# Kernel tuning notes

Hardware: AMD Instinct MI355X
Metric: run time of the kernel (lower is better)

Reference implementation:

```python
import jax, jax.numpy as jnp
import numpy as np

N_P, N_I, DIM = 30, 40, 6
W_I, C1, C2, LAM = 0.7, 1.5, 1.5, 0.3
EPS = 1e-8


def _decode(pos):
    # pos: [P, 6] -> per-particle fusion weights via pairwise softmax
    e = jnp.exp(pos[:, :4])
    fg_s = e[:, 0] + e[:, 1] + EPS
    bg_s = e[:, 2] + e[:, 3] + EPS
    return e[:, 0] / fg_s, e[:, 1] / fg_s, e[:, 2] / bg_s, e[:, 3] / bg_s


def _fitness(pos, rgb, dep, mask, r_dep):
    # rgb, dep, mask, r_dep: [H, W]; pos: [P, 6] -> scores [P]
    rgb_fg, dep_fg, rgb_bg, dep_bg = _decode(pos)
    mn = mask - mask.mean()
    mn_norm = jnp.linalg.norm(mn) + EPS
    fg = rgb_fg[:, None, None] * rgb + dep_fg[:, None, None] * dep   # [P,H,W]
    bg = rgb_bg[:, None, None] * rgb + dep_bg[:, None, None] * dep
    fused = mask * fg + (1.0 - mask) * bg
    fn = fused - fused.mean(axis=(1, 2), keepdims=True)
    fn_norm = jnp.sqrt((fn * fn).sum(axis=(1, 2)))
    ncc = (fn * mn).sum(axis=(1, 2)) / (fn_norm * mn_norm + EPS)
    pen_fg = ((1.0 - r_dep) * mask).mean()
    pen_bg = ((1.0 - r_dep) * (1.0 - mask)).mean()
    rel_pen = dep_fg * pen_fg + dep_bg * pen_bg
    return ncc - LAM * rel_pen


def _pso(rgb, dep, mask, r_dep):
    # Deterministic PSO with fixed RNG key; inputs are [H, W] maps.
    key = jax.random.key(42)
    k_pos, k_vel, k_r1, k_r2 = jax.random.split(key, 4)
    pos = jax.random.uniform(k_pos, (N_P, DIM), minval=-2.0, maxval=2.0)
    vel = jax.random.uniform(k_vel, (N_P, DIM), minval=-0.5, maxval=0.5)
    r1s = jax.random.uniform(k_r1, (N_I, N_P, DIM))
    r2s = jax.random.uniform(k_r2, (N_I, N_P, DIM))

    pb_pos = pos
    pb_fit = _fitness(pos, rgb, dep, mask, r_dep)
    gi = jnp.argmax(pb_fit)
    gb_pos = pb_pos[gi]
    gb_fit = pb_fit[gi]

    def step(carry, rs):
        pos, vel, pb_pos, pb_fit, gb_pos, gb_fit = carry
        r1, r2 = rs
        vel = W_I * vel + C1 * r1 * (pb_pos - pos) + C2 * r2 * (gb_pos - pos)
        pos = jnp.clip(pos + vel, -3.0, 3.0)
        fit = _fitness(pos, rgb, dep, mask, r_dep)
        better = fit > pb_fit
        pb_pos = jnp.where(better[:, None], pos, pb_pos)
        pb_fit = jnp.where(better, fit, pb_fit)
        bi = jnp.argmax(pb_fit)
        improve = pb_fit[bi] > gb_fit
        gb_pos = jnp.where(improve, pb_pos[bi], gb_pos)
        gb_fit = jnp.where(improve, pb_fit[bi], gb_fit)
        return (pos, vel, pb_pos, pb_fit, gb_pos, gb_fit), None

    (pos, vel, pb_pos, pb_fit, gb_pos, gb_fit), _ = jax.lax.scan(
        step, (pos, vel, pb_pos, pb_fit, gb_pos, gb_fit), (r1s, r2s))
    rgb_fg, dep_fg, rgb_bg, dep_bg = _decode(gb_pos[None, :])
    return rgb_fg[0], dep_fg[0], rgb_bg[0], dep_bg[0]


def _cos_sim(feat, proto):
    # feat [B,C,H,W], proto [B,C] -> [B,H,W]; matches F.normalize (clamp_min eps)
    p = proto / jnp.maximum(jnp.linalg.norm(proto, axis=1, keepdims=True), 1e-12)
    fnorm = jnp.maximum(jnp.sqrt((feat * feat).sum(axis=1, keepdims=True)), 1e-12)
    f = feat / fnorm
    return jnp.einsum('bchw,bc->bhw', f, p)


def setup_inputs() -> dict:
    key = jax.random.key(0)
    ks = jax.random.split(key, 10)
    B, C, H, W = 8, 256, 64, 64
    return {
        'f_rgb': jax.random.normal(ks[0], (B, C, H, W), dtype=jnp.float32),
        'f_depth': jax.random.normal(ks[1], (B, C, H, W), dtype=jnp.float32),
        'r_rgb': jax.random.uniform(ks[2], (B, 1, H, W), dtype=jnp.float32),
        'r_depth': jax.random.uniform(ks[3], (B, 1, H, W), dtype=jnp.float32),
        'proto_rgb': jax.random.normal(ks[4], (B, C), dtype=jnp.float32),
        'proto_dep': jax.random.normal(ks[5], (B, C), dtype=jnp.float32),
        'query_mask': jax.random.uniform(ks[6], (B, 1, H, W), dtype=jnp.float32),
        'conv_w': jax.random.normal(ks[7], (C, C), dtype=jnp.float32) * 0.05,
        'bn_gamma': jax.random.uniform(ks[8], (C,), dtype=jnp.float32),
        'bn_beta': jax.random.normal(ks[9], (C,), dtype=jnp.float32) * 0.1,
        'bn_mean': jnp.zeros((C,), dtype=jnp.float32),
        'bn_var': jnp.ones((C,), dtype=jnp.float32),
    }


def reference(f_rgb, f_depth, r_rgb, r_depth, proto_rgb, proto_dep, query_mask,
              conv_w, bn_gamma, bn_beta, bn_mean, bn_var):
    # cosine similarity maps [B,H,W]
    rgb_sim = _cos_sim(f_rgb, proto_rgb)
    dep_sim = _cos_sim(f_depth, proto_dep)

    # PSO operates on detached batch-mean maps (torch .detach().mean(0).cpu())
    sg = jax.lax.stop_gradient
    np_rgb = sg(rgb_sim).mean(axis=0)                 # [H,W]
    np_dep = sg(dep_sim).mean(axis=0)                 # [H,W]
    np_mask = sg(query_mask)[:, 0].mean(axis=0)       # mask already at (H,W): nearest interp is identity
    np_r_dep = sg(r_depth)[:, 0].mean(axis=0)
    rgb_fg, dep_fg, rgb_bg, dep_bg = _pso(np_rgb, np_dep, np_mask, np_r_dep)

    f_fg = rgb_fg * f_rgb + dep_fg * f_depth
    f_bg = rgb_bg * f_rgb + dep_bg * f_depth
    proxy = jax.nn.sigmoid((rgb_sim + dep_sim)[:, None] * 3.0)   # [B,1,H,W]
    f_fused = proxy * f_fg + (1.0 - proxy) * f_bg

    # post_proj: 1x1 conv (no bias) -> BN (eval) -> ReLU
    y = jnp.einsum('oc,bchw->bohw', conv_w, f_fused)
    inv = bn_gamma / jnp.sqrt(bn_var + 1e-5)
    y = y * inv[None, :, None, None] + (bn_beta - bn_mean * inv)[None, :, None, None]
    return jax.nn.relu(y)
```

## Files before the change

### kernel.cpp

```cpp
#include <hip/hip_runtime.h>
#include <stdint.h>
#include <float.h>

static constexpr size_t WS_SIM_RGB = 4096;
static constexpr size_t WS_SIM_DEP = 36864;
static constexpr size_t WS_NPMAPS  = 69632;
static constexpr size_t WS_SYNC    = 86048;
static constexpr size_t WS_RNG     = 90112;

typedef short short8 __attribute__((ext_vector_type(8)));
typedef float f32x4 __attribute__((ext_vector_type(4)));

static constexpr uint32_t SYNC_MAGIC = 0x5A17C0DEu;

__device__ __forceinline__ uint32_t pack_bf2(float a, float b) {
  uint32_t ua = __float_as_uint(a), ub = __float_as_uint(b);
  uint32_t ra = (ua + 0x7fffu + ((ua >> 16) & 1u)) >> 16;
  uint32_t rb = (ub + 0x7fffu + ((ub >> 16) & 1u)) >> 16;
  return (ra & 0xffffu) | (rb << 16);
}

__device__ __forceinline__ void threefry2x32(uint32_t k0, uint32_t k1,
                                             uint32_t c0, uint32_t c1,
                                             uint32_t& o0, uint32_t& o1) {
  uint32_t ks2 = k0 ^ k1 ^ 0x1BD11BDAu;
  uint32_t x0 = c0 + k0;
  uint32_t x1 = c1 + k1;
#define TF_ROUND(r) { x0 += x1; x1 = (x1 << (r)) | (x1 >> (32 - (r))); x1 ^= x0; }
  TF_ROUND(13) TF_ROUND(15) TF_ROUND(26) TF_ROUND(6)
  x0 += k1;  x1 += ks2 + 1u;
  TF_ROUND(17) TF_ROUND(29) TF_ROUND(16) TF_ROUND(24)
  x0 += ks2; x1 += k0 + 2u;
  TF_ROUND(13) TF_ROUND(15) TF_ROUND(26) TF_ROUND(6)
  x0 += k0;  x1 += k1 + 3u;
  TF_ROUND(17) TF_ROUND(29) TF_ROUND(16) TF_ROUND(24)
  x0 += k1;  x1 += ks2 + 4u;
  TF_ROUND(13) TF_ROUND(15) TF_ROUND(26) TF_ROUND(6)
  x0 += ks2; x1 += k0 + 5u;
#undef TF_ROUND
  o0 = x0; o1 = x1;
}

__device__ __forceinline__ float tf_u01(uint32_t k0, uint32_t k1, uint32_t idx) {
  uint32_t o0, o1;
  threefry2x32(k0, k1, 0u, idx, o0, o1);
  uint32_t bits = o0 ^ o1;
  uint32_t fb = (bits >> 9) | 0x3F800000u;
  return __uint_as_float(fb) - 1.0f;
}

__global__ __launch_bounds__(256) void sim_kernel(
    const float* __restrict__ f_rgb, const float* __restrict__ f_dep,
    const float* __restrict__ proto_rgb, const float* __restrict__ proto_dep,
    float* __restrict__ sim_rgb, float* __restrict__ sim_dep) {
  int tid = threadIdx.x;
  int bm = blockIdx.y;
  int b = bm >> 1, mo = bm & 1;
  const float* f  = mo ? f_dep : f_rgb;
  const float* pr = mo ? proto_dep : proto_rgb;
  float* sim = mo ? sim_dep : sim_rgb;
  __shared__ float shp[256];
  __shared__ float wsum[4];
  float pv = pr[b * 256 + tid];
  float ss0 = pv * pv;
#pragma unroll
  for (int off = 32; off > 0; off >>= 1) ss0 += __shfl_xor(ss0, off, 64);
  if ((tid & 63) == 0) wsum[tid >> 6] = ss0;
  __syncthreads();
  float nrm = fmaxf(sqrtf(wsum[0] + wsum[1] + wsum[2] + wsum[3]), 1e-12f);
  shp[tid] = pv / nrm;
  __syncthreads();
  int p = blockIdx.x * 256 + tid;
  const float* base = f + (size_t)b * 256 * 4096 + p;
  float dot = 0.f, ss = 0.f;
#pragma unroll 8
  for (int c = 0; c < 256; ++c) {
    float x = base[(size_t)c * 4096];
    dot += x * shp[c];
    ss  += x * x;
  }
  float fn = fmaxf(sqrtf(ss), 1e-12f);
  sim[b * 4096 + p] = dot / fn;
}

__global__ __launch_bounds__(256) void npmaps_kernel(
    const float* __restrict__ sim_rgb, const float* __restrict__ sim_dep,
    const float* __restrict__ qmask, const float* __restrict__ r_dep,
    float* __restrict__ npm) {
  int i = blockIdx.x * 256 + threadIdx.x;
  float sr = 0.f, sd = 0.f, sm = 0.f, sq = 0.f;
#pragma unroll
  for (int b = 0; b < 8; ++b) {
    sr += sim_rgb[b * 4096 + i];
    sd += sim_dep[b * 4096 + i];
    sm += qmask[b * 4096 + i];
    sq += r_dep[b * 4096 + i];
  }
  npm[i]          = sr * 0.125f;
  npm[4096 + i]   = sd * 0.125f;
  npm[8192 + i]   = sm * 0.125f;
  npm[12288 + i]  = sq * 0.125f;
}

__global__ __launch_bounds__(256) void rng_kernel(float* __restrict__ rng) {
  int g = blockIdx.x * 256 + threadIdx.x;
  if (g >= 14760) return;
  int kind; uint32_t splitIdx, ctr, dst;
  if (g < 180) {
    kind = 0; splitIdx = 0; ctr = (uint32_t)g; dst = (uint32_t)g;
  } else if (g < 360) {
    kind = 1; splitIdx = 1; ctr = (uint32_t)(g - 180); dst = (uint32_t)g;
  } else if (g < 7560) {
    uint32_t c = (uint32_t)(g - 360);
    kind = 2; splitIdx = 2; ctr = c;
    uint32_t t = c / 180u, rem = c % 180u, p = rem / 6u, d = rem % 6u;
    dst = 360u + t * 360u + p * 12u + d;
  } else {
    uint32_t c = (uint32_t)(g - 7560);
    kind = 3; splitIdx = 3; ctr = c;
    uint32_t t = c / 180u, rem = c % 180u, p = rem / 6u, d = rem % 6u;
    dst = 360u + t * 360u + p * 12u + 6u + d;
  }
  uint32_t k0, k1;
  threefry2x32(0u, 42u, 0u, splitIdx, k0, k1);
  float u = tf_u01(k0, k1, ctr);
  float v;
  if (kind == 0)      v = fmaxf(-2.0f, u * 4.0f - 2.0f);
  else if (kind == 1) v = fmaxf(-0.5f, u - 0.5f);
  else                v = u;
  rng[dst] = v;
}

__device__ __forceinline__ float pso_fitness_fast(const float pos[6],
    const float S[4], const float G[16], const float V[4],
    float mn_norm, float pen_fg, float pen_bg) {
  float e0 = __expf(pos[0]), e1 = __expf(pos[1]);
  float e2 = __expf(pos[2]), e3 = __expf(pos[3]);
  float rf = __builtin_amdgcn_rcpf(e0 + e1 + 1e-8f);
  float rb = __builtin_amdgcn_rcpf(e2 + e3 + 1e-8f);
  float w[4] = {e0 * rf, e1 * rf, e2 * rb, e3 * rb};
  float num = 0.f, mus = 0.f;
#pragma unroll
  for (int k = 0; k < 4; ++k) { num += w[k] * V[k]; mus += w[k] * S[k]; }
  float q = 0.f;
#pragma unroll
  for (int j = 0; j < 4; ++j)
#pragma unroll
    for (int k = 0; k < 4; ++k) q += w[j] * G[j * 4 + k] * w[k];
  float fn2 = fmaxf(q - mus * mus * (1.f / 4096.f), 0.f);
  float den = __builtin_amdgcn_sqrtf(fn2) * mn_norm + 1e-8f;
  float ncc = num * __builtin_amdgcn_rcpf(den);
  return ncc - 0.3f * (w[1] * pen_fg + w[3] * pen_bg);
}

__device__ __forceinline__ float wavemax_lo32(float v) {
  int x = __float_as_int(v);
#define DPP_STEP(ctrl) { \
    int y = __builtin_amdgcn_update_dpp(x, x, ctrl, 0xf, 0xf, false); \
    x = __float_as_int(fmaxf(__int_as_float(x), __int_as_float(y))); }
  DPP_STEP(0x128)
  DPP_STEP(0x124)
  DPP_STEP(0x122)
  DPP_STEP(0x121)
#undef DPP_STEP
  float r0 = __int_as_float(__builtin_amdgcn_readlane(x, 0));
  float r1 = __int_as_float(__builtin_amdgcn_readlane(x, 16));
  return fmaxf(r0, r1);
}

__global__ __launch_bounds__(256, 4) void mega_kernel(
    const float* __restrict__ f_rgb, const float* __restrict__ f_dep,
    const float* __restrict__ sim_rgb, const float* __restrict__ sim_dep,
    const float* __restrict__ npm, const float* __restrict__ rng,
    const float* __restrict__ W,
    const float* __restrict__ bn_g, const float* __restrict__ bn_b,
    const float* __restrict__ bn_m, const float* __restrict__ bn_v,
    uint32_t* __restrict__ sync, float* __restrict__ out) {
  __shared__ __align__(16) uint32_t smem[4736];
  const int tid = threadIdx.x;
  const int bid = blockIdx.x;

  if (bid == 0) {
    float* colf = (float*)smem;
    float* res1 = colf + 17 * 257;
    float* res2 = res1 + 17;
    float* sst  = res2 + 5;
    const float* np_rgb  = npm;
    const float* np_dep  = npm + 4096;
    const float* np_mask = npm + 8192;
    const float* np_rdep = npm + 12288;
    {
      float acc[17];
#pragma unroll
      for (int k = 0; k < 17; ++k) acc[k] = 0.f;
      for (int i = tid; i < 4096; i += 256) {
        float m = np_mask[i], r = np_rgb[i], d = np_dep[i], q = np_rdep[i];
        float om = 1.f - m;
        float M1 = m * r, M2 = m * d, M3 = om * r, M4 = om * d;
        acc[0] += m;
        acc[1] += M1; acc[2] += M2; acc[3] += M3; acc[4] += M4;
        acc[5] += M1 * M1; acc[6] += M1 * M2; acc[7] += M1 * M3; acc[8] += M1 * M4;
        acc[9] += M2 * M2; acc[10] += M2 * M3; acc[11] += M2 * M4;
        acc[12] += M3 * M3; acc[13] += M3 * M4; acc[14] += M4 * M4;
        float oq = 1.f - q;
        acc[15] += oq * m; acc[16] += oq * om;
      }
#pragma unroll
      for (int k = 0; k < 17; ++k) colf[k * 257 + tid] = acc[k];
      __syncthreads();
      if (tid < 17) { float s = 0.f; for (int i = 0; i < 256; ++i) s += colf[tid * 257 + i]; res1[tid] = s; }
      __syncthreads();
      float mask_mean = res1[0] * (1.f / 4096.f);
      float a2[5] = {0.f, 0.f, 0.f, 0.f, 0.f};
      for (int i = tid; i < 4096; i += 256) {
        float m = np_mask[i], r = np_rgb[i], d = np_dep[i];
        float om = 1.f - m;
        float mn = m - mask_mean;
        a2[0] += m * r * mn; a2[1] += m * d * mn;
        a2[2] += om * r * mn; a2[3] += om * d * mn;
        a2[4] += mn * mn;
      }
      __syncthreads();
#pragma unroll
      for (int k = 0; k < 5; ++k) colf[k * 257 + tid] = a2[k];
      __syncthreads();
      if (tid < 5) { float s = 0.f; for (int i = 0; i < 256; ++i) s += colf[tid * 257 + i]; res2[tid] = s; }
      __syncthreads();
      if (tid == 0) {
        sst[0] = res1[1]; sst[1] = res1[2]; sst[2] = res1[3]; sst[3] = res1[4];
        float G11 = res1[5], G12 = res1[6], G13 = res1[7], G14 = res1[8];
        float G22 = res1[9], G23 = res1[10], G24 = res1[11];
        float G33 = res1[12], G34 = res1[13], G44 = res1[14];
        float Gf[16] = {G11, G12, G13, G14,  G12, G22, G23, G24,
                        G13, G23, G33, G34,  G14, G24, G34, G44};
        for (int k = 0; k < 16; ++k) sst[4 + k] = Gf[k];
        sst[20] = res2[0]; sst[21] = res2[1]; sst[22] = res2[2]; sst[23] = res2[3];
        sst[24] = sqrtf(res2[4]) + 1e-8f;
        sst[25] = res1[15] * (1.f / 4096.f);
        sst[26] = res1[16] * (1.f / 4096.f);
      }
      __syncthreads();
    }
    if (tid >= 64) return;
    int lane = tid;
    bool act = lane < 30;
    float S[4], G[16], V[4];
#pragma unroll
    for (int k = 0; k < 4; ++k) S[k] = sst[k];
#pragma unroll
    for (int k = 0; k < 16; ++k) G[k] = sst[4 + k];
#pragma unroll
    for (int k = 0; k < 4; ++k) V[k] = sst[20 + k];
    float mn_norm = sst[24], pen_fg = sst[25], pen_bg = sst[26];

    float pos[6], vel[6], pbp[6];
#pragma unroll
    for (int d = 0; d < 6; ++d) { pos[d] = 0.f; vel[d] = 0.f; }
    if (act) {
#pragma unroll
      for (int d = 0; d < 6; ++d) {
        pos[d] = rng[lane * 6 + d];
        vel[d] = rng[180 + lane * 6 + d];
      }
    }
#pragma unroll
    for (int d = 0; d < 6; ++d) pbp[d] = pos[d];

    float f0 = pso_fitness_fast(pos, S, G, V, mn_norm, pen_fg, pen_bg);
    float pbf = act ? f0 : -FLT_MAX;

    float gbf = wavemax_lo32(pbf);
    float gb[6];
    {
      unsigned long long mm = __ballot(pbf == gbf);
      int bl = __ffsll(mm) - 1;
#pragma unroll
      for (int d = 0; d < 6; ++d)
        gb[d] = __int_as_float(__builtin_amdgcn_readlane(__float_as_int(pbp[d]), bl));
    }

    const float* rbase = rng + 360;
    float4 A0, A1, A2, B0, B1, B2;
    {
      const float4* p0 = (const float4*)(rbase + lane * 12);
      A0 = p0[0]; A1 = p0[1]; A2 = p0[2];
      const float4* p1 = (const float4*)(rbase + 360 + lane * 12);
      B0 = p1[0]; B1 = p1[1]; B2 = p1[2];
    }

#define PSO_ITER(R0, R1, R2, TNEXT) { \
    float r1v[6] = {R0.x, R0.y, R0.z, R0.w, R1.x, R1.y}; \
    float r2v[6] = {R1.z, R1.w, R2.x, R2.y, R2.z, R2.w}; \
    const float4* pf = (const float4*)(rbase + (TNEXT) * 360 + lane * 12); \
    R0 = pf[0]; R1 = pf[1]; R2 = pf[2]; \
    _Pragma("unroll") \
    for (int d = 0; d < 6; ++d) { \
      vel[d] = 0.7f * vel[d] + 1.5f * r1v[d] * (pbp[d] - pos[d]) \
                             + 1.5f * r2v[d] * (gb[d] - pos[d]); \
      pos[d] = fmaxf(-3.0f, fminf(pos[d] + vel[d], 3.0f)); \
    } \
    float f = pso_fitness_fast(pos, S, G, V, mn_norm, pen_fg, pen_bg); \
    if (act && f > pbf) { \
      pbf = f; \
      _Pragma("unroll") for (int d = 0; d < 6; ++d) pbp[d] = pos[d]; \
    } \
    float maxv = wavemax_lo32(pbf); \
    if (maxv > gbf) {     \
      unsigned long long mm = __ballot(pbf == maxv); \
      int bl = __ffsll(mm) - 1; \
      gbf = maxv; \
      _Pragma("unroll") for (int d = 0; d < 6; ++d) \
        gb[d] = __int_as_float(__builtin_amdgcn_readlane(__float_as_int(pbp[d]), bl)); \
    } \
  }

    for (int k = 0; k < 20; ++k) {
      PSO_ITER(A0, A1, A2, 2 * k + 2)
      PSO_ITER(B0, B1, B2, 2 * k + 3)
    }
#undef PSO_ITER

    if (lane == 0) {
      float e0 = expf(gb[0]), e1 = expf(gb[1]), e2 = expf(gb[2]), e3 = expf(gb[3]);
      float fgs = e0 + e1 + 1e-8f, bgs = e2 + e3 + 1e-8f;
      uint32_t u0 = __float_as_uint(e0 / fgs);
      uint32_t u1 = __float_as_uint(e1 / fgs);
      uint32_t u2 = __float_as_uint(e2 / bgs);
      uint32_t u3 = __float_as_uint(e3 / bgs);
      atomicExch(&sync[0], u0);
      atomicExch(&sync[1], u1);
      atomicExch(&sync[2], u2);
      atomicExch(&sync[3], u3);
      __threadfence();
      atomicExch(&sync[4], u0 ^ u1 ^ u2 ^ u3 ^ SYNC_MAGIC);
    }
    return;
  }

  uint32_t* As = smem;
  uint32_t* BR = smem + 2560;
  uint32_t* BD = smem + 3648;
  const int gi = bid - 1;
  const int t0 = gi;
  const int t1 = (gi == 0) ? 1023 : -1;

  const int n4 = (tid & 15) * 4, kp = tid >> 4;
  const int am = tid & 127, kh = tid >> 7;
  const int lane = tid & 63, wv = tid >> 6;
  const int wm = wv >> 1, wn = wv & 1;
  const int lg = lane >> 4, ln = lane & 15;

  float pa = 0.f, pb_ = 0.f, pc_ = 0.f, pd_ = 0.f;
  bool have = false;

  for (int pass = 0; pass < 2; ++pass) {
    const int t = pass ? t1 : t0;
    if (t < 0) break;
    const int b = t >> 7, rem = t & 127, mt = rem >> 6, nt = rem & 63;
    const int m0 = mt * 128, n0 = nt * 64;
    const size_t fb = (size_t)b << 20;
    const float* frb = f_rgb + fb + n0 + n4;
    const float* fdb = f_dep + fb + n0 + n4;
    const float* wrow = W + (size_t)(m0 + am) * 256 + kh * 16;

    f32x4 accR[4][2], accD[4][2];
#pragma unroll
    for (int i = 0; i < 4; ++i)
#pragma unroll
      for (int j = 0; j < 2; ++j) { accR[i][j] = (f32x4)0.f; accD[i][j] = (f32x4)0.f; }

    for (int s8 = 0; s8 < 8; ++s8) {
      const int k0 = s8 * 32;
      {
        const size_t ko = (size_t)(k0 + 2 * kp) * 4096;
        const f32x4 r0 = *(const f32x4*)(frb + ko);
        const f32x4 r1 = *(const f32x4*)(frb + ko + 4096);
        const f32x4 d0 = *(const f32x4*)(fdb + ko);
        const f32x4 d1 = *(const f32x4*)(fdb + ko + 4096);
#pragma unroll
        for (int i2 = 0; i2 < 4; ++i2) {
          BR[(n4 + i2) * 17 + kp] = pack_bf2(r0[i2], r1[i2]);
          BD[(n4 + i2) * 17 + kp] = pack_bf2(d0[i2], d1[i2]);
        }
        const f32x4 w0 = *(const f32x4*)(wrow + k0);
        const f32x4 w1 = *(const f32x4*)(wrow + k0 + 4);
        const f32x4 w2 = *(const f32x4*)(wrow + k0 + 8);
        const f32x4 w3 = *(const f32x4*)(wrow + k0 + 12);
        uint32_t* ap = &As[am * 20 + kh * 8];
        ap[0] = pack_bf2(w0[0], w0[1]); ap[1] = pack_bf2(w0[2], w0[3]);
        ap[2] = pack_bf2(w1[0], w1[1]); ap[3] = pack_bf2(w1[2], w1[3]);
        ap[4] = pack_bf2(w2[0], w2[1]); ap[5] = pack_bf2(w2[2], w2[3]);
        ap[6] = pack_bf2(w3[0], w3[1]); ap[7] = pack_bf2(w3[2], w3[3]);
      }
      __syncthreads();
      short8 af[4], bfr[2], bfd[2];
#pragma unroll
      for (int i = 0; i < 4; ++i) {
        int m = wm * 64 + i * 16 + ln;
        float4 tq = *(const float4*)(&As[m * 20 + lg * 4]);
        af[i] = *(short8*)&tq;
      }
#pragma unroll
      for (int j = 0; j < 2; ++j) {
        int n = wn * 32 + j * 16 + ln;
        const uint32_t* bp = &BR[n * 17 + lg * 4];
        union { uint32_t w[4]; short8 v; } u;
        u.w[0] = bp[0]; u.w[1] = bp[1]; u.w[2] = bp[2]; u.w[3] = bp[3];
        bfr[j] = u.v;
        const uint32_t* dp = &BD[n * 17 + lg * 4];
        union { uint32_t w[4]; short8 v; } ud;
        ud.w[0] = dp[0]; ud.w[1] = dp[1]; ud.w[2] = dp[2]; ud.w[3] = dp[3];
        bfd[j] = ud.v;
      }
#pragma unroll
      for (int i = 0; i < 4; ++i)
#pragma unroll
        for (int j = 0; j < 2; ++j) {
          accR[i][j] = __builtin_amdgcn_mfma_f32_16x16x32_bf16(af[i], bfr[j], accR[i][j], 0, 0, 0);
          accD[i][j] = __builtin_amdgcn_mfma_f32_16x16x32_bf16(af[i], bfd[j], accD[i][j], 0, 0, 0);
        }
      __syncthreads();
    }

    if (!have) {
      if (tid == 0) {
        uint32_t a, b2, c, d, k;
        for (;;) {
          k  = atomicAdd(&sync[4], 0u);
          a  = atomicAdd(&sync[0], 0u);
          b2 = atomicAdd(&sync[1], 0u);
          c  = atomicAdd(&sync[2], 0u);
          d  = atomicAdd(&sync[3], 0u);
          if (k == (a ^ b2 ^ c ^ d ^ SYNC_MAGIC)) break;
          __builtin_amdgcn_s_sleep(32);
        }
        smem[0] = a; smem[1] = b2; smem[2] = c; smem[3] = d;
      }
      __syncthreads();
      pa  = __uint_as_float(smem[0]);
      pb_ = __uint_as_float(smem[1]);
      pc_ = __uint_as_float(smem[2]);
      pd_ = __uint_as_float(smem[3]);
      have = true;
      __syncthreads();
    }

    float abx0, aby0, abx1, aby1;
    {
      int nj0 = n0 + wn * 32 + ln;
      int nj1 = nj0 + 16;
      float s0 = sim_rgb[b * 4096 + nj0] + sim_dep[b * 4096 + nj0];
      float s1 = sim_rgb[b * 4096 + nj1] + sim_dep[b * 4096 + nj1];
      float pr0 = 1.f / (1.f + expf(-3.f * s0));
      float pr1 = 1.f / (1.f + expf(-3.f * s1));
      abx0 = pr0 * pa + (1.f - pr0) * pc_;  aby0 = pr0 * pb_ + (1.f - pr0) * pd_;
      abx1 = pr1 * pa + (1.f - pr1) * pc_;  aby1 = pr1 * pb_ + (1.f - pr1) * pd_;
    }
#pragma unroll
    for (int i = 0; i < 4; ++i) {
#pragma unroll
      for (int r = 0; r < 4; ++r) {
        int m = m0 + wm * 64 + i * 16 + lg * 4 + r;
        float inv = bn_g[m] / sqrtf(bn_v[m] + 1e-5f);
        float sh = bn_b[m] - bn_m[m] * inv;
        float* orow = out + ((size_t)(b * 256 + m)) * 4096 + n0 + wn * 32 + ln;
        float v0 = abx0 * accR[i][0][r] + aby0 * accD[i][0][r];
        float v1 = abx1 * accR[i][1][r] + aby1 * accD[i][1][r];
        orow[0]  = fmaxf(v0 * inv + sh, 0.f);
        orow[16] = fmaxf(v1 * inv + sh, 0.f);
      }
    }
    if (pass == 0 && t1 >= 0) __syncthreads();
  }
}

extern "C" void kernel_launch(void* const* d_in, const int* in_sizes, int n_in,
                              void* d_out, int out_size, void* d_ws, size_t ws_size,
                              hipStream_t stream) {
  (void)in_sizes; (void)n_in; (void)out_size; (void)ws_size;
  const float* f_rgb     = (const float*)d_in[0];
  const float* f_depth   = (const float*)d_in[1];
  const float* r_depth   = (const float*)d_in[3];
  const float* proto_rgb = (const float*)d_in[4];
  const float* proto_dep = (const float*)d_in[5];
  const float* qmask     = (const float*)d_in[6];
  const float* conv_w    = (const float*)d_in[7];
  const float* bn_g      = (const float*)d_in[8];
  const float* bn_b      = (const float*)d_in[9];
  const float* bn_m      = (const float*)d_in[10];
  const float* bn_v      = (const float*)d_in[11];
  float* out = (float*)d_out;
  float* ws  = (float*)d_ws;

  float* sim_rgb = ws + WS_SIM_RGB;
  float* sim_dep = ws + WS_SIM_DEP;
  float* npm     = ws + WS_NPMAPS;
  uint32_t* sync = (uint32_t*)(ws + WS_SYNC);
  float* rng     = ws + WS_RNG;

  rng_kernel<<<dim3(58), dim3(256), 0, stream>>>(rng);
  sim_kernel<<<dim3(16, 16), dim3(256), 0, stream>>>(f_rgb, f_depth, proto_rgb,
                                                     proto_dep, sim_rgb, sim_dep);
  npmaps_kernel<<<dim3(16), dim3(256), 0, stream>>>(sim_rgb, sim_dep, qmask, r_depth, npm);
  mega_kernel<<<dim3(1024), dim3(256), 0, stream>>>(f_rgb, f_depth, sim_rgb, sim_dep,
                                                    npm, rng, conv_w,
                                                    bn_g, bn_b, bn_m, bn_v, sync, out);
}
```

Measured before the change: 68.47 us.

## Fold RNG generation into mega kernel block 0 and rebalance the extra GEMM tile

Removes the separate rng_kernel launch. Block 0 of the mega kernel now generates the threefry random numbers itself, looping 58 times per thread, before running the PSO. Block 0 also computes GEMM tile 1023 after finishing the PSO, instead of block 1 computing two tiles. This saves a kernel launch and makes the tile loop single-pass, but it puts the serial RNG work and a full tile on block 0's critical path. It also reads and writes the same rng buffer through two __restrict__ pointers.

```diff
diff --git a/kernel.cpp b/kernel.cpp
--- a/kernel.cpp
+++ b/kernel.cpp
@@ -102,35 +102,6 @@
   npm[12288 + i]  = sq * 0.125f;
 }
 
-__global__ __launch_bounds__(256) void rng_kernel(float* __restrict__ rng) {
-  int g = blockIdx.x * 256 + threadIdx.x;
-  if (g >= 14760) return;
-  int kind; uint32_t splitIdx, ctr, dst;
-  if (g < 180) {
-    kind = 0; splitIdx = 0; ctr = (uint32_t)g; dst = (uint32_t)g;
-  } else if (g < 360) {
-    kind = 1; splitIdx = 1; ctr = (uint32_t)(g - 180); dst = (uint32_t)g;
-  } else if (g < 7560) {
-    uint32_t c = (uint32_t)(g - 360);
-    kind = 2; splitIdx = 2; ctr = c;
-    uint32_t t = c / 180u, rem = c % 180u, p = rem / 6u, d = rem % 6u;
-    dst = 360u + t * 360u + p * 12u + d;
-  } else {
-    uint32_t c = (uint32_t)(g - 7560);
-    kind = 3; splitIdx = 3; ctr = c;
-    uint32_t t = c / 180u, rem = c % 180u, p = rem / 6u, d = rem % 6u;
-    dst = 360u + t * 360u + p * 12u + 6u + d;
-  }
-  uint32_t k0, k1;
-  threefry2x32(0u, 42u, 0u, splitIdx, k0, k1);
-  float u = tf_u01(k0, k1, ctr);
-  float v;
-  if (kind == 0)      v = fmaxf(-2.0f, u * 4.0f - 2.0f);
-  else if (kind == 1) v = fmaxf(-0.5f, u - 0.5f);
-  else                v = u;
-  rng[dst] = v;
-}
-
 __device__ __forceinline__ float pso_fitness_fast(const float pos[6],
     const float S[4], const float G[16], const float V[4],
     float mn_norm, float pen_fg, float pen_bg) {
@@ -171,8 +142,8 @@
 __global__ __launch_bounds__(256, 4) void mega_kernel(
     const float* __restrict__ f_rgb, const float* __restrict__ f_dep,
     const float* __restrict__ sim_rgb, const float* __restrict__ sim_dep,
-    const float* __restrict__ npm, const float* __restrict__ rng,
-    const float* __restrict__ W,
+    const float* __restrict__ npm, const float* __restrict__ rng_in,
+    float* __restrict__ rng_out, const float* __restrict__ W,
     const float* __restrict__ bn_g, const float* __restrict__ bn_b,
     const float* __restrict__ bn_m, const float* __restrict__ bn_v,
     uint32_t* __restrict__ sync, float* __restrict__ out) {
@@ -181,6 +152,35 @@
   const int bid = blockIdx.x;
 
   if (bid == 0) {
+    for (int j = 0; j < 58; ++j) {
+      int g = tid + 256 * j;
+      if (g < 14760) {
+        int kind; uint32_t splitIdx, ctr, dst;
+        if (g < 180)      { kind = 0; splitIdx = 0; ctr = (uint32_t)g; dst = (uint32_t)g; }
+        else if (g < 360) { kind = 1; splitIdx = 1; ctr = (uint32_t)(g - 180); dst = (uint32_t)g; }
+        else if (g < 7560) {
+          uint32_t c = (uint32_t)(g - 360);
+          kind = 2; splitIdx = 2; ctr = c;
+          uint32_t t = c / 180u, rem = c % 180u, p = rem / 6u, d = rem % 6u;
+          dst = 360u + t * 360u + p * 12u + d;
+        } else {
+          uint32_t c = (uint32_t)(g - 7560);
+          kind = 3; splitIdx = 3; ctr = c;
+          uint32_t t = c / 180u, rem = c % 180u, p = rem / 6u, d = rem % 6u;
+          dst = 360u + t * 360u + p * 12u + 6u + d;
+        }
+        uint32_t k0, k1;
+        threefry2x32(0u, 42u, 0u, splitIdx, k0, k1);
+        float u = tf_u01(k0, k1, ctr);
+        float v;
+        if (kind == 0)      v = fmaxf(-2.0f, u * 4.0f - 2.0f);
+        else if (kind == 1) v = fmaxf(-0.5f, u - 0.5f);
+        else                v = u;
+        rng_out[dst] = v;
+      }
+    }
+    __syncthreads();
+
     float* colf = (float*)smem;
     float* res1 = colf + 17 * 257;
     float* res2 = res1 + 17;
@@ -241,52 +241,53 @@
       }
       __syncthreads();
     }
-    if (tid >= 64) return;
-    int lane = tid;
-    bool act = lane < 30;
-    float S[4], G[16], V[4];
-#pragma unroll
-    for (int k = 0; k < 4; ++k) S[k] = sst[k];
-#pragma unroll
-    for (int k = 0; k < 16; ++k) G[k] = sst[4 + k];
-#pragma unroll
-    for (int k = 0; k < 4; ++k) V[k] = sst[20 + k];
-    float mn_norm = sst[24], pen_fg = sst[25], pen_bg = sst[26];
-
-    float pos[6], vel[6], pbp[6];
-#pragma unroll
-    for (int d = 0; d < 6; ++d) { pos[d] = 0.f; vel[d] = 0.f; }
-    if (act) {
-#pragma unroll
-      for (int d = 0; d < 6; ++d) {
-        pos[d] = rng[lane * 6 + d];
-        vel[d] = rng[180 + lane * 6 + d];
-      }
-    }
-#pragma unroll
-    for (int d = 0; d < 6; ++d) pbp[d] = pos[d];
-
-    float f0 = pso_fitness_fast(pos, S, G, V, mn_norm, pen_fg, pen_bg);
-    float pbf = act ? f0 : -FLT_MAX;
-
-    float gbf = wavemax_lo32(pbf);
-    float gb[6];
-    {
-      unsigned long long mm = __ballot(pbf == gbf);
-      int bl = __ffsll(mm) - 1;
-#pragma unroll
-      for (int d = 0; d < 6; ++d)
-        gb[d] = __int_as_float(__builtin_amdgcn_readlane(__float_as_int(pbp[d]), bl));
-    }
-
-    const float* rbase = rng + 360;
-    float4 A0, A1, A2, B0, B1, B2;
-    {
-      const float4* p0 = (const float4*)(rbase + lane * 12);
-      A0 = p0[0]; A1 = p0[1]; A2 = p0[2];
-      const float4* p1 = (const float4*)(rbase + 360 + lane * 12);
-      B0 = p1[0]; B1 = p1[1]; B2 = p1[2];
-    }
+
+    if (tid < 64) {
+      int lane = tid;
+      bool act = lane < 30;
+      float S[4], G[16], V[4];
+#pragma unroll
+      for (int k = 0; k < 4; ++k) S[k] = sst[k];
+#pragma unroll
+      for (int k = 0; k < 16; ++k) G[k] = sst[4 + k];
+#pragma unroll
+      for (int k = 0; k < 4; ++k) V[k] = sst[20 + k];
+      float mn_norm = sst[24], pen_fg = sst[25], pen_bg = sst[26];
+
+      float pos[6], vel[6], pbp[6];
+#pragma unroll
+      for (int d = 0; d < 6; ++d) { pos[d] = 0.f; vel[d] = 0.f; }
+      if (act) {
+#pragma unroll
+        for (int d = 0; d < 6; ++d) {
+          pos[d] = rng_in[lane * 6 + d];
+          vel[d] = rng_in[180 + lane * 6 + d];
+        }
+      }
+#pragma unroll
+      for (int d = 0; d < 6; ++d) pbp[d] = pos[d];
+
+      float f0 = pso_fitness_fast(pos, S, G, V, mn_norm, pen_fg, pen_bg);
+      float pbf = act ? f0 : -FLT_MAX;
+
+      float gbf = wavemax_lo32(pbf);
+      float gb[6];
+      {
+        unsigned long long mm = __ballot(pbf == gbf);
+        int bl = __ffsll(mm) - 1;
+#pragma unroll
+        for (int d = 0; d < 6; ++d)
+          gb[d] = __int_as_float(__builtin_amdgcn_readlane(__float_as_int(pbp[d]), bl));
+      }
+
+      const float* rbase = rng_in + 360;
+      float4 A0, A1, A2, B0, B1, B2;
+      {
+        const float4* p0 = (const float4*)(rbase + lane * 12);
+        A0 = p0[0]; A1 = p0[1]; A2 = p0[2];
+        const float4* p1 = (const float4*)(rbase + 360 + lane * 12);
+        B0 = p1[0]; B1 = p1[1]; B2 = p1[2];
+      }
 
 #define PSO_ITER(R0, R1, R2, TNEXT) { \
     float r1v[6] = {R0.x, R0.y, R0.z, R0.w, R1.x, R1.y}; \
@@ -314,35 +315,34 @@
     } \
   }
 
-    for (int k = 0; k < 20; ++k) {
-      PSO_ITER(A0, A1, A2, 2 * k + 2)
-      PSO_ITER(B0, B1, B2, 2 * k + 3)
-    }
+      for (int k = 0; k < 20; ++k) {
+        PSO_ITER(A0, A1, A2, 2 * k + 2)
+        PSO_ITER(B0, B1, B2, 2 * k + 3)
+      }
 #undef PSO_ITER
 
-    if (lane == 0) {
-      float e0 = expf(gb[0]), e1 = expf(gb[1]), e2 = expf(gb[2]), e3 = expf(gb[3]);
-      float fgs = e0 + e1 + 1e-8f, bgs = e2 + e3 + 1e-8f;
-      uint32_t u0 = __float_as_uint(e0 / fgs);
-      uint32_t u1 = __float_as_uint(e1 / fgs);
-      uint32_t u2 = __float_as_uint(e2 / bgs);
-      uint32_t u3 = __float_as_uint(e3 / bgs);
-      atomicExch(&sync[0], u0);
-      atomicExch(&sync[1], u1);
-      atomicExch(&sync[2], u2);
-      atomicExch(&sync[3], u3);
-      __threadfence();
-      atomicExch(&sync[4], u0 ^ u1 ^ u2 ^ u3 ^ SYNC_MAGIC);
-    }
-    return;
+      if (lane == 0) {
+        float e0 = expf(gb[0]), e1 = expf(gb[1]), e2 = expf(gb[2]), e3 = expf(gb[3]);
+        float fgs = e0 + e1 + 1e-8f, bgs = e2 + e3 + 1e-8f;
+        uint32_t u0 = __float_as_uint(e0 / fgs);
+        uint32_t u1 = __float_as_uint(e1 / fgs);
+        uint32_t u2 = __float_as_uint(e2 / bgs);
+        uint32_t u3 = __float_as_uint(e3 / bgs);
+        atomicExch(&sync[0], u0);
+        atomicExch(&sync[1], u1);
+        atomicExch(&sync[2], u2);
+        atomicExch(&sync[3], u3);
+        __threadfence();
+        atomicExch(&sync[4], u0 ^ u1 ^ u2 ^ u3 ^ SYNC_MAGIC);
+      }
+    }
+    __syncthreads();
   }
 
   uint32_t* As = smem;
   uint32_t* BR = smem + 2560;
   uint32_t* BD = smem + 3648;
-  const int gi = bid - 1;
-  const int t0 = gi;
-  const int t1 = (gi == 0) ? 1023 : -1;
+  const int t = (bid == 0) ? 1023 : (bid - 1);
 
   const int n4 = (tid & 15) * 4, kp = tid >> 4;
   const int am = tid & 127, kh = tid >> 7;
@@ -350,127 +350,118 @@
   const int wm = wv >> 1, wn = wv & 1;
   const int lg = lane >> 4, ln = lane & 15;
 
-  float pa = 0.f, pb_ = 0.f, pc_ = 0.f, pd_ = 0.f;
-  bool have = false;
-
-  for (int pass = 0; pass < 2; ++pass) {
-    const int t = pass ? t1 : t0;
-    if (t < 0) break;
-    const int b = t >> 7, rem = t & 127, mt = rem >> 6, nt = rem & 63;
-    const int m0 = mt * 128, n0 = nt * 64;
-    const size_t fb = (size_t)b << 20;
-    const float* frb = f_rgb + fb + n0 + n4;
-    const float* fdb = f_dep + fb + n0 + n4;
-    const float* wrow = W + (size_t)(m0 + am) * 256 + kh * 16;
-
-    f32x4 accR[4][2], accD[4][2];
+  const int b = t >> 7, rem = t & 127, mt = rem >> 6, nt = rem & 63;
+  const int m0 = mt * 128, n0 = nt * 64;
+  const size_t fb = (size_t)b << 20;
+  const float* frb = f_rgb + fb + n0 + n4;
+  const float* fdb = f_dep + fb + n0 + n4;
+  const float* wrow = W + (size_t)(m0 + am) * 256 + kh * 16;
+
+  f32x4 accR[4][2], accD[4][2];
+#pragma unroll
+  for (int i = 0; i < 4; ++i)
+#pragma unroll
+    for (int j = 0; j < 2; ++j) { accR[i][j] = (f32x4)0.f; accD[i][j] = (f32x4)0.f; }
+
+  for (int s8 = 0; s8 < 8; ++s8) {
+    const int k0 = s8 * 32;
+    {
+      const size_t ko = (size_t)(k0 + 2 * kp) * 4096;
+      const f32x4 r0 = *(const f32x4*)(frb + ko);
+      const f32x4 r1 = *(const f32x4*)(frb + ko + 4096);
+      const f32x4 d0 = *(const f32x4*)(fdb + ko);
+      const f32x4 d1 = *(const f32x4*)(fdb + ko + 4096);
+#pragma unroll
+      for (int i2 = 0; i2 < 4; ++i2) {
+        BR[(n4 + i2) * 17 + kp] = pack_bf2(r0[i2], r1[i2]);
+        BD[(n4 + i2) * 17 + kp] = pack_bf2(d0[i2], d1[i2]);
+      }
+      const f32x4 w0 = *(const f32x4*)(wrow + k0);
+      const f32x4 w1 = *(const f32x4*)(wrow + k0 + 4);
+      const f32x4 w2 = *(const f32x4*)(wrow + k0 + 8);
+      const f32x4 w3 = *(const f32x4*)(wrow + k0 + 12);
+      uint32_t* ap = &As[am * 20 + kh * 8];
+      ap[0] = pack_bf2(w0[0], w0[1]); ap[1] = pack_bf2(w0[2], w0[3]);
+      ap[2] = pack_bf2(w1[0], w1[1]); ap[3] = pack_bf2(w1[2], w1[3]);
+      ap[4] = pack_bf2(w2[0], w2[1]); ap[5] = pack_bf2(w2[2], w2[3]);
+      ap[6] = pack_bf2(w3[0], w3[1]); ap[7] = pack_bf2(w3[2], w3[3]);
+    }
+    __syncthreads();
+    short8 af[4], bfr[2], bfd[2];
+#pragma unroll
+    for (int i = 0; i < 4; ++i) {
+      int m = wm * 64 + i * 16 + ln;
+      float4 tq = *(const float4*)(&As[m * 20 + lg * 4]);
+      af[i] = *(short8*)&tq;
+    }
+#pragma unroll
+    for (int j = 0; j < 2; ++j) {
+      int n = wn * 32 + j * 16 + ln;
+      const uint32_t* bp = &BR[n * 17 + lg * 4];
+      union { uint32_t w[4]; short8 v; } u;
+      u.w[0] = bp[0]; u.w[1] = bp[1]; u.w[2] = bp[2]; u.w[3] = bp[3];
+      bfr[j] = u.v;
+      const uint32_t* dp = &BD[n * 17 + lg * 4];
+      union { uint32_t w[4]; short8 v; } ud;
+      ud.w[0] = dp[0]; ud.w[1] = dp[1]; ud.w[2] = dp[2]; ud.w[3] = dp[3];
+      bfd[j] = ud.v;
+    }
 #pragma unroll
     for (int i = 0; i < 4; ++i)
 #pragma unroll
-      for (int j = 0; j < 2; ++j) { accR[i][j] = (f32x4)0.f; accD[i][j] = (f32x4)0.f; }
-
-    for (int s8 = 0; s8 < 8; ++s8) {
-      const int k0 = s8 * 32;
-      {
-        const size_t ko = (size_t)(k0 + 2 * kp) * 4096;
-        const f32x4 r0 = *(const f32x4*)(frb + ko);
-        const f32x4 r1 = *(const f32x4*)(frb + ko + 4096);
-        const f32x4 d0 = *(const f32x4*)(fdb + ko);
-        const f32x4 d1 = *(const f32x4*)(fdb + ko + 4096);
-#pragma unroll
-        for (int i2 = 0; i2 < 4; ++i2) {
-          BR[(n4 + i2) * 17 + kp] = pack_bf2(r0[i2], r1[i2]);
-          BD[(n4 + i2) * 17 + kp] = pack_bf2(d0[i2], d1[i2]);
-        }
-        const f32x4 w0 = *(const f32x4*)(wrow + k0);
-        const f32x4 w1 = *(const f32x4*)(wrow + k0 + 4);
-        const f32x4 w2 = *(const f32x4*)(wrow + k0 + 8);
-        const f32x4 w3 = *(const f32x4*)(wrow + k0 + 12);
-        uint32_t* ap = &As[am * 20 + kh * 8];
-        ap[0] = pack_bf2(w0[0], w0[1]); ap[1] = pack_bf2(w0[2], w0[3]);
-        ap[2] = pack_bf2(w1[0], w1[1]); ap[3] = pack_bf2(w1[2], w1[3]);
-        ap[4] = pack_bf2(w2[0], w2[1]); ap[5] = pack_bf2(w2[2], w2[3]);
-        ap[6] = pack_bf2(w3[0], w3[1]); ap[7] = pack_bf2(w3[2], w3[3]);
-      }
-      __syncthreads();
-      short8 af[4], bfr[2], bfd[2];
-#pragma unroll
-      for (int i = 0; i < 4; ++i) {
-        int m = wm * 64 + i * 16 + ln;
-        float4 tq = *(const float4*)(&As[m * 20 + lg * 4]);
-        af[i] = *(short8*)&tq;
-      }
-#pragma unroll
       for (int j = 0; j < 2; ++j) {
-        int n = wn * 32 + j * 16 + ln;
-        const uint32_t* bp = &BR[n * 17 + lg * 4];
-        union { uint32_t w[4]; short8 v; } u;
-        u.w[0] = bp[0]; u.w[1] = bp[1]; u.w[2] = bp[2]; u.w[3] = bp[3];
-        bfr[j] = u.v;
-        const uint32_t* dp = &BD[n * 17 + lg * 4];
-        union { uint32_t w[4]; short8 v; } ud;
-        ud.w[0] = dp[0]; ud.w[1] = dp[1]; ud.w[2] = dp[2]; ud.w[3] = dp[3];
-        bfd[j] = ud.v;
-      }
-#pragma unroll
-      for (int i = 0; i < 4; ++i)
-#pragma unroll
-        for (int j = 0; j < 2; ++j) {
-          accR[i][j] = __builtin_amdgcn_mfma_f32_16x16x32_bf16(af[i], bfr[j], accR[i][j], 0, 0, 0);
-          accD[i][j] = __builtin_amdgcn_mfma_f32_16x16x32_bf16(af[i], bfd[j], accD[i][j], 0, 0, 0);
-        }
-      __syncthreads();
-    }
-
-    if (!have) {
-      if (tid == 0) {
-        uint32_t a, b2, c, d, k;
-        for (;;) {
-          k  = atomicAdd(&sync[4], 0u);
-          a  = atomicAdd(&sync[0], 0u);
-          b2 = atomicAdd(&sync[1], 0u);
-          c  = atomicAdd(&sync[2], 0u);
-          d  = atomicAdd(&sync[3], 0u);
-          if (k == (a ^ b2 ^ c ^ d ^ SYNC_MAGIC)) break;
-          __builtin_amdgcn_s_sleep(32);
-        }
-        smem[0] = a; smem[1] = b2; smem[2] = c; smem[3] = d;
-      }
-      __syncthreads();
-      pa  = __uint_as_float(smem[0]);
-      pb_ = __uint_as_float(smem[1]);
-      pc_ = __uint_as_float(smem[2]);
-      pd_ = __uint_as_float(smem[3]);
-      have = true;
-      __syncthreads();
-    }
-
-    float abx0, aby0, abx1, aby1;
-    {
-      int nj0 = n0 + wn * 32 + ln;
-      int nj1 = nj0 + 16;
-      float s0 = sim_rgb[b * 4096 + nj0] + sim_dep[b * 4096 + nj0];
-      float s1 = sim_rgb[b * 4096 + nj1] + sim_dep[b * 4096 + nj1];
-      float pr0 = 1.f / (1.f + expf(-3.f * s0));
-      float pr1 = 1.f / (1.f + expf(-3.f * s1));
-      abx0 = pr0 * pa + (1.f - pr0) * pc_;  aby0 = pr0 * pb_ + (1.f - pr0) * pd_;
-      abx1 = pr1 * pa + (1.f - pr1) * pc_;  aby1 = pr1 * pb_ + (1.f - pr1) * pd_;
-    }
-#pragma unroll
-    for (int i = 0; i < 4; ++i) {
-#pragma unroll
-      for (int r = 0; r < 4; ++r) {
-        int m = m0 + wm * 64 + i * 16 + lg * 4 + r;
-        float inv = bn_g[m] / sqrtf(bn_v[m] + 1e-5f);
-        float sh = bn_b[m] - bn_m[m] * inv;
-        float* orow = out + ((size_t)(b * 256 + m)) * 4096 + n0 + wn * 32 + ln;
-        float v0 = abx0 * accR[i][0][r] + aby0 * accD[i][0][r];
-        float v1 = abx1 * accR[i][1][r] + aby1 * accD[i][1][r];
-        orow[0]  = fmaxf(v0 * inv + sh, 0.f);
-        orow[16] = fmaxf(v1 * inv + sh, 0.f);
-      }
-    }
-    if (pass == 0 && t1 >= 0) __syncthreads();
+        accR[i][j] = __builtin_amdgcn_mfma_f32_16x16x32_bf16(af[i], bfr[j], accR[i][j], 0, 0, 0);
+        accD[i][j] = __builtin_amdgcn_mfma_f32_16x16x32_bf16(af[i], bfd[j], accD[i][j], 0, 0, 0);
+      }
+    __syncthreads();
+  }
+
+  {
+    if (tid == 0) {
+      uint32_t a, b2, c, d, k;
+      for (;;) {
+        k  = atomicAdd(&sync[4], 0u);
+        a  = atomicAdd(&sync[0], 0u);
+        b2 = atomicAdd(&sync[1], 0u);
+        c  = atomicAdd(&sync[2], 0u);
+        d  = atomicAdd(&sync[3], 0u);
+        if (k == (a ^ b2 ^ c ^ d ^ SYNC_MAGIC)) break;
+        __builtin_amdgcn_s_sleep(32);
+      }
+      __threadfence();
+      smem[0] = a; smem[1] = b2; smem[2] = c; smem[3] = d;
+    }
+    __syncthreads();
+  }
+  const float pa  = __uint_as_float(smem[0]);
+  const float pb_ = __uint_as_float(smem[1]);
+  const float pc_ = __uint_as_float(smem[2]);
+  const float pd_ = __uint_as_float(smem[3]);
+
+  float abx0, aby0, abx1, aby1;
+  {
+    int nj0 = n0 + wn * 32 + ln;
+    int nj1 = nj0 + 16;
+    float s0 = sim_rgb[b * 4096 + nj0] + sim_dep[b * 4096 + nj0];
+    float s1 = sim_rgb[b * 4096 + nj1] + sim_dep[b * 4096 + nj1];
+    float pr0 = 1.f / (1.f + expf(-3.f * s0));
+    float pr1 = 1.f / (1.f + expf(-3.f * s1));
+    abx0 = pr0 * pa + (1.f - pr0) * pc_;  aby0 = pr0 * pb_ + (1.f - pr0) * pd_;
+    abx1 = pr1 * pa + (1.f - pr1) * pc_;  aby1 = pr1 * pb_ + (1.f - pr1) * pd_;
+  }
+#pragma unroll
+  for (int i = 0; i < 4; ++i) {
+#pragma unroll
+    for (int r = 0; r < 4; ++r) {
+      int m = m0 + wm * 64 + i * 16 + lg * 4 + r;
+      float inv = bn_g[m] / sqrtf(bn_v[m] + 1e-5f);
+      float sh = bn_b[m] - bn_m[m] * inv;
+      float* orow = out + ((size_t)(b * 256 + m)) * 4096 + n0 + wn * 32 + ln;
+      float v0 = abx0 * accR[i][0][r] + aby0 * accD[i][0][r];
+      float v1 = abx1 * accR[i][1][r] + aby1 * accD[i][1][r];
+      orow[0]  = fmaxf(v0 * inv + sh, 0.f);
+      orow[16] = fmaxf(v1 * inv + sh, 0.f);
+    }
   }
 }
 
@@ -498,11 +489,10 @@
   uint32_t* sync = (uint32_t*)(ws + WS_SYNC);
   float* rng     = ws + WS_RNG;
 
-  rng_kernel<<<dim3(58), dim3(256), 0, stream>>>(rng);
   sim_kernel<<<dim3(16, 16), dim3(256), 0, stream>>>(f_rgb, f_depth, proto_rgb,
                                                      proto_dep, sim_rgb, sim_dep);
   npmaps_kernel<<<dim3(16), dim3(256), 0, stream>>>(sim_rgb, sim_dep, qmask, r_depth, npm);
   mega_kernel<<<dim3(1024), dim3(256), 0, stream>>>(f_rgb, f_depth, sim_rgb, sim_dep,
-                                                    npm, rng, conv_w,
+                                                    npm, rng, rng, conv_w,
                                                     bn_g, bn_b, bn_m, bn_v, sync, out);
 }
```

New measurement: 124.8 us. +82.2%, slower.
